# Performance work log

Measured on AMD Instinct MI355X. Metric: run time of the kernel, lower is better.

The kernel has to match this reference:

```python
import jax, jax.numpy as jnp
import numpy as np

B, T, S, D, H, F = 4, 1024, 1024, 1024, 16, 4096
NEG = jnp.float32(-1e9)


def _ln(x, g, b):
    m = jnp.mean(x, axis=-1, keepdims=True)
    v = jnp.mean((x - m) ** 2, axis=-1, keepdims=True)
    return (x - m) * jax.lax.rsqrt(v + 1e-5) * g + b


def _mha(q, k, v, wq, bq, wk, bk, wv, bv, wo, bo, scale, mask, causal, sbias):
    Bq, Tq, Dq = q.shape
    Sk = k.shape[1]
    dk = Dq // H
    Q = (q @ wq.T + bq).reshape(Bq, Tq, H, dk).transpose(0, 2, 1, 3)  # [B,H,T,dk]
    K = (k @ wk.T + bk).reshape(Bq, Sk, H, dk).transpose(0, 2, 1, 3)  # [B,H,S,dk]
    V = (v @ wv.T + bv).reshape(Bq, Sk, H, dk).transpose(0, 2, 1, 3)
    s = jnp.einsum('bhtd,bhsd->bhts', Q, K) / jnp.sqrt(jnp.float32(dk))
    if sbias is not None:
        s = s + scale * sbias[:, None, None, :]
    if mask is not None:
        s = jnp.where(mask == 0, NEG, s)
    if causal is not None:
        s = jnp.where(causal == 0, NEG, s)
    a = jax.nn.softmax(s, axis=-1)
    o = jnp.einsum('bhts,bhsd->bhtd', a, V).transpose(0, 2, 1, 3).reshape(Bq, Tq, Dq)
    return o @ wo.T + bo


def setup_inputs():
    key = jax.random.key(0)
    ks = jax.random.split(key, 16)
    r = lambda i, shape, s=0.02: jax.random.normal(ks[i], shape, dtype=jnp.float32) * s
    z = lambda *shape: jnp.zeros(shape, jnp.float32)
    o = lambda *shape: jnp.ones(shape, jnp.float32)
    inp = dict(
        x=r(0, (B, T, D), 1.0),
        memory=r(1, (B, S, D), 1.0),
        sentence_bias=r(2, (B, S), 1.0),
        trg_mask=jnp.ones((B, 1, 1, T), jnp.int32),
        trg_causal_mask=jnp.tril(jnp.ones((T, T), jnp.int32))[None, None],
        src_mask=jnp.ones((B, 1, 1, S), jnp.int32),
        sa_wq=r(3, (D, D)), sa_bq=z(D), sa_wk=r(4, (D, D)), sa_bk=z(D),
        sa_wv=r(5, (D, D)), sa_bv=z(D), sa_wo=r(6, (D, D)), sa_bo=z(D),
        sa_scale=jnp.float32(0.1),
        ca_wq=r(7, (D, D)), ca_bq=z(D), ca_wk=r(8, (D, D)), ca_bk=z(D),
        ca_wv=r(9, (D, D)), ca_bv=z(D), ca_wo=r(10, (D, D)), ca_bo=z(D),
        ca_scale=jnp.float32(0.1),
        ln1_g=o(D), ln1_b=z(D), ln2_g=o(D), ln2_b=z(D), ln3_g=o(D), ln3_b=z(D),
        ffn_w1=r(11, (F, D)), ffn_b1=z(F), ffn_w2=r(12, (D, F)), ffn_b2=z(D),
    )
    return inp


def reference(x, memory, trg_mask, trg_causal_mask, src_mask, sentence_bias,
              sa_wq, sa_bq, sa_wk, sa_bk, sa_wv, sa_bv, sa_wo, sa_bo, sa_scale,
              ca_wq, ca_bq, ca_wk, ca_bk, ca_wv, ca_bv, ca_wo, ca_bo, ca_scale,
              ln1_g, ln1_b, ln2_g, ln2_b, ln3_g, ln3_b,
              ffn_w1, ffn_b1, ffn_w2, ffn_b2):
    # Faithful quirk: Q comes from normed x, K/V from raw residual stream.
    x = x + _mha(_ln(x, ln1_g, ln1_b), x, x,
                 sa_wq, sa_bq, sa_wk, sa_bk, sa_wv, sa_bv, sa_wo, sa_bo,
                 sa_scale, trg_mask, trg_causal_mask, None)
    x = x + _mha(_ln(x, ln2_g, ln2_b), memory, memory,
                 ca_wq, ca_bq, ca_wk, ca_bk, ca_wv, ca_bv, ca_wo, ca_bo,
                 ca_scale, src_mask, None, sentence_bias)
    h = _ln(x, ln3_g, ln3_b)
    x = x + (jax.nn.relu(h @ ffn_w1.T + ffn_b1) @ ffn_w2.T + ffn_b2)
    return x
```

## Files before the change

kernel.cpp:

```cpp
#include <hip/hip_runtime.h>
#include <hip/hip_bf16.h>
#include <cmath>
#include <stdint.h>

typedef __hip_bfloat16 bf16;
typedef __attribute__((ext_vector_type(8))) __bf16 bf16x8;
typedef __attribute__((ext_vector_type(8))) unsigned short u16x8;
typedef __attribute__((ext_vector_type(4))) float f32x4;

__device__ __forceinline__ void gld16(const void* g, const void* l)
{
    __builtin_amdgcn_global_load_lds(
        (const __attribute__((address_space(1))) unsigned int*)(unsigned long long)g,
        (__attribute__((address_space(3))) unsigned int*)(unsigned int)(unsigned long long)l,
        16, 0, 0);
}

struct CvtSrcs { const float* p[24]; };

__global__ __launch_bounds__(256) void cvt_all(
    CvtSrcs s, bf16* __restrict__ dst,
    const float* __restrict__ lg, const float* __restrict__ lb,
    bf16* __restrict__ lnout)
{
    const int t = threadIdx.x;
    const int i = (blockIdx.x * 256 + t) * 8;
    const int seg = i >> 20;
    const float* sp = s.p[seg] + (i & 1048575);
    const float4 a = *(const float4*)(sp);
    const float4 b = *(const float4*)(sp + 4);
    const float v[8] = {a.x, a.y, a.z, a.w, b.x, b.y, b.z, b.w};
    bf16 tmp[8];
#pragma unroll
    for (int j = 0; j < 8; ++j) tmp[j] = __float2bfloat16(v[j]);
    *(uint4*)(dst + i) = *(const uint4*)tmp;

    if (seg < 4) {
        float s1 = 0.f, s2 = 0.f;
#pragma unroll
        for (int j = 0; j < 8; ++j) { s1 += v[j]; s2 += v[j] * v[j]; }
#pragma unroll
        for (int off = 32; off > 0; off >>= 1) {
            s1 += __shfl_xor(s1, off, 64);
            s2 += __shfl_xor(s2, off, 64);
        }
        __shared__ float r1[4], r2[4];
        const int w = t >> 6;
        if ((t & 63) == 0) { r1[w] = s1; r2[w] = s2; }
        __syncthreads();
        const int rw = (w >> 1) * 2;
        s1 = r1[rw] + r1[rw + 1];
        s2 = r2[rw] + r2[rw + 1];
        const float mean = s1 * (1.f / 1024.f);
        const float var  = s2 * (1.f / 1024.f) - mean * mean;
        const float rstd = rsqrtf(var + 1e-5f);
        bf16 lt[8];
        const int c0 = i & 1023;
#pragma unroll
        for (int j = 0; j < 8; ++j)
            lt[j] = __float2bfloat16((v[j] - mean) * rstd * lg[c0 + j] + lb[c0 + j]);
        *(uint4*)(lnout + i) = *(const uint4*)lt;
    }
}

enum {
    EPI_QSCALE = 0,
    EPI_KV = 1,
    EPI_RELU = 2,
    EPI_RES_F32_F32OUT = 3,
    EPI_PART = 4
};

template <int EPI>
__device__ __forceinline__ void gemm_bt_body(
    unsigned short* __restrict__ sAp, unsigned short* __restrict__ sBp,
    const bf16* __restrict__ A, const bf16* __restrict__ W,
    const float* __restrict__ bias, const float* __restrict__ bias2,
    const float* __restrict__ res, void* __restrict__ out,
    int N, int Kiter, int Kstride, int bx)
{
    const int t  = threadIdx.x;
    const int l  = t & 63;
    const int w  = t >> 6;
    const int wv = w * 64;
    const int wr = w >> 1;
    const int wc = w & 1;
    const int lm = l & 15;
    const int kq = l >> 4;
    const int rx = lm & 7;

    const int xcd = bx & 7;
    const int ib  = bx >> 3;
    const int bm  = xcd * 4 + (ib & 3);
    const int bn  = ib >> 2;

    const bf16* gA = A + (size_t)(bm * 128 + (t >> 3)) * Kstride
                       + ((t & 7) ^ ((t >> 3) & 7)) * 8;
    const bf16* gB = W + (size_t)(bn * 64 + (t >> 3)) * Kstride
                       + ((t & 7) ^ ((t >> 3) & 7)) * 8;

#define SQA_B(slot, kt, j)                                      \
    gld16(gA + (size_t)((j) * 32) * Kstride + (kt) * 64,        \
          sAp + (slot) * 8192 + ((j) * 256 + wv) * 8)
#define SQB_B(slot, kt, j)                                      \
    gld16(gB + (size_t)((j) * 32) * Kstride + (kt) * 64,        \
          sBp + (slot) * 4096 + ((j) * 256 + wv) * 8)

    bf16x8 af[4][2], bg[2][2];

#define READ_A_B(s_, mh, kk)                                                \
    do {                                                                    \
        _Pragma("unroll")                                                   \
        for (int m2 = 0; m2 < 2; ++m2) {                                    \
            const int mi = (mh) * 2 + m2;                                   \
            const int lr = wr * 64 + mi * 16 + lm;                          \
            const int sl = (((kk) << 2) | kq) ^ rx;                         \
            af[mi][kk] = __builtin_bit_cast(bf16x8,                         \
                *(const u16x8*)(sAp + (s_) * 8192 + lr * 64 + sl * 8));     \
        }                                                                   \
    } while (0)
#define READ_B_B(s_, kk)                                                    \
    do {                                                                    \
        _Pragma("unroll")                                                   \
        for (int ni = 0; ni < 2; ++ni) {                                    \
            const int lr = wc * 32 + ni * 16 + lm;                          \
            const int sl = (((kk) << 2) | kq) ^ rx;                         \
            bg[ni][kk] = __builtin_bit_cast(bf16x8,                         \
                *(const u16x8*)(sBp + (s_) * 4096 + lr * 64 + sl * 8));     \
        }                                                                   \
    } while (0)
#define MFMA_PH_B(mh, kk)                                                   \
    do {                                                                    \
        __builtin_amdgcn_s_setprio(1);                                      \
        _Pragma("unroll")                                                   \
        for (int m2 = 0; m2 < 2; ++m2)                                      \
            _Pragma("unroll")                                               \
            for (int ni = 0; ni < 2; ++ni)                                  \
                acc[(mh) * 2 + m2][ni] =                                    \
                    __builtin_amdgcn_mfma_f32_16x16x32_bf16(                \
                        af[(mh) * 2 + m2][kk], bg[ni][kk],                  \
                        acc[(mh) * 2 + m2][ni], 0, 0, 0);                   \
        __builtin_amdgcn_s_setprio(0);                                      \
    } while (0)
#define BARRIER_B() do { __builtin_amdgcn_s_barrier();                      \
                         __builtin_amdgcn_sched_barrier(0); } while (0)
#define WAITV0_B() asm volatile("s_waitcnt vmcnt(0)" ::: "memory")

    f32x4 acc[4][2] = {};
    const int NT = Kiter >> 6;

    SQB_B(0, 0, 0); SQB_B(0, 0, 1);
    SQA_B(0, 0, 0); SQA_B(0, 0, 1); SQA_B(0, 0, 2); SQA_B(0, 0, 3);

    for (int tt = 0; tt < NT; ++tt) {
        const int s = tt & 1, d = s ^ 1, kn = tt + 1;
        WAITV0_B(); BARRIER_B();
        if (kn < NT) {
            SQB_B(d, kn, 0); SQB_B(d, kn, 1);
            SQA_B(d, kn, 0); SQA_B(d, kn, 1); SQA_B(d, kn, 2); SQA_B(d, kn, 3);
        }
        READ_A_B(s, 0, 0); READ_B_B(s, 0);
        MFMA_PH_B(0, 0);
        READ_A_B(s, 1, 0);
        MFMA_PH_B(1, 0);
        READ_A_B(s, 1, 1); READ_B_B(s, 1);
        MFMA_PH_B(1, 1);
        READ_A_B(s, 0, 1);
        MFMA_PH_B(0, 1);
    }
#undef SQA_B
#undef SQB_B
#undef READ_A_B
#undef READ_B_B
#undef MFMA_PH_B
#undef BARRIER_B
#undef WAITV0_B

    if (EPI == EPI_RELU) {
        __syncthreads();
        unsigned short* scr = sBp + w * 2048;
#pragma unroll
        for (int ni = 0; ni < 2; ++ni) {
            const int col = bn * 64 + wc * 32 + ni * 16 + lm;
            const float bv = bias[col];
            const int c  = ni * 2 + (lm >> 3);
            const int ci = lm & 7;
#pragma unroll
            for (int mi = 0; mi < 4; ++mi)
#pragma unroll
                for (int r = 0; r < 4; ++r) {
                    const int row = mi * 16 + kq * 4 + r;
                    const float v = fmaxf(acc[mi][ni][r] + bv, 0.f);
                    scr[row * 32 + ((c ^ (row & 3)) * 8) + ci] =
                        __builtin_bit_cast(unsigned short, (__bf16)v);
                }
        }
        asm volatile("s_waitcnt lgkmcnt(0)" ::: "memory");
#pragma unroll
        for (int it = 0; it < 4; ++it) {
            const int row = it * 16 + (l >> 2);
            const int lc  = l & 3;
            const u16x8 vv = *(const u16x8*)&scr[row * 32 + ((lc ^ (row & 3)) * 8)];
            const int Crow = bm * 128 + wr * 64 + row;
            const int Ccol = bn * 64 + wc * 32 + lc * 8;
            *(u16x8*)((bf16*)out + (size_t)Crow * N + Ccol) = vv;
        }
        return;
    }

#pragma unroll
    for (int ni = 0; ni < 2; ++ni) {
        const int col = bn * 64 + wc * 32 + ni * 16 + lm;
        float bv = 0.f;
        if (EPI == EPI_KV) bv = (col < 1024) ? bias[col] : bias2[col - 1024];
        else bv = bias[col];
#pragma unroll
        for (int mi = 0; mi < 4; ++mi) {
#pragma unroll
            for (int r = 0; r < 4; ++r) {
                const int row = bm * 128 + wr * 64 + mi * 16 + kq * 4 + r;
                float v = acc[mi][ni][r] + bv;
                if (EPI == EPI_QSCALE) v *= 0.125f;
                if (EPI == EPI_KV) {
                    if (col < 1024) {
                        ((bf16*)out)[(size_t)row * 1024 + col] = __float2bfloat16(v);
                    } else {
                        const int ch = col - 1024;
                        const size_t idx = (size_t)4 * 1048576 +
                            ((size_t)((row >> 10) * 16 + (ch >> 6)) * 64 + (ch & 63)) * 1024
                            + (row & 1023);
                        ((bf16*)out)[idx] = __float2bfloat16(v);
                    }
                } else if (EPI == EPI_RES_F32_F32OUT) {
                    const size_t idx = (size_t)row * N + col;
                    ((float*)out)[idx] = v + res[idx];
                } else {
                    ((bf16*)out)[(size_t)row * N + col] = __float2bfloat16(v);
                }
            }
        }
    }
}

template <int EPI>
__global__ __launch_bounds__(256, 3) void gemm_bt(
    const bf16* __restrict__ A, const bf16* __restrict__ W,
    const float* __restrict__ bias, const float* __restrict__ bias2,
    const float* __restrict__ res, void* __restrict__ out,
    int M, int N, int Kiter, int Kstride)
{
    __shared__ __align__(16) unsigned short sA[2 * 128 * 64];
    __shared__ __align__(16) unsigned short sB[2 * 64 * 64];
    gemm_bt_body<EPI>(sA, sB, A, W, bias, bias2, res, out,
                      N, Kiter, Kstride, blockIdx.x);
}

__global__ __launch_bounds__(256, 3) void qkv_fused(
    const bf16* __restrict__ Aq, const bf16* __restrict__ Wq,
    const float* __restrict__ bq, bf16* __restrict__ Qb,
    const bf16* __restrict__ Akv, const bf16* __restrict__ Wkv,
    const float* __restrict__ bk, const float* __restrict__ bv,
    bf16* __restrict__ Kb)
{
    __shared__ __align__(16) unsigned short sA[2 * 128 * 64];
    __shared__ __align__(16) unsigned short sB[2 * 64 * 64];
    const int bx = blockIdx.x;
    if (bx < 512)
        gemm_bt_body<EPI_QSCALE>(sA, sB, Aq, Wq, bq, nullptr, nullptr, Qb,
                                 1024, 1024, 1024, bx);
    else
        gemm_bt_body<EPI_KV>(sA, sB, Akv, Wkv, bk, bv, nullptr, Kb,
                             2048, 1024, 1024, bx - 512);
}

template <bool CAUSAL, bool SBIAS>
__global__ __launch_bounds__(256, 2) void flash_attn(
    const bf16* __restrict__ Q, const bf16* __restrict__ K,
    const bf16* __restrict__ Vt, bf16* __restrict__ O,
    const float* __restrict__ sbias, const float* __restrict__ scale_ptr)
{
    __shared__ __align__(16) unsigned short sK[2][64 * 64];
    __shared__ __align__(16) unsigned short sV[2][64 * 64];
    __shared__ __align__(16) unsigned short sP[4 * 32 * 72];

    const int t  = threadIdx.x;
    const int l  = t & 63;
    const int w  = t >> 6;
    const int wv = w * 64;
    const int lm = l & 15;
    const int kq = l >> 4;

    const int bh = blockIdx.x & 63;
    const int qb = blockIdx.x >> 6;
    const int h  = bh & 15;
    const int b  = bh >> 4;

    const int tb = qb * 128 + w * 32;
    const size_t qrow0 = (size_t)(b * 1024 + tb) * 1024 + h * 64;

    bf16x8 qf[2][2];
#pragma unroll
    for (int mi = 0; mi < 2; ++mi)
#pragma unroll
        for (int kk = 0; kk < 2; ++kk)
            qf[mi][kk] = __builtin_bit_cast(bf16x8,
                *(const u16x8*)(Q + qrow0 + (size_t)(mi * 16 + lm) * 1024 + kk * 32 + kq * 8));

    float cs = 0.f; const float* sb = nullptr;
    if (SBIAS) { cs = scale_ptr[0]; sb = sbias + b * 1024; }

    const bf16* gK = K  + (size_t)(b * 1024 + (t >> 3)) * 1024 + h * 64
                   + ((t & 7) ^ ((t >> 3) & 7)) * 8;
    const bf16* gV = Vt + (size_t)((b * 16 + h) * 64 + (t >> 3)) * 1024
                   + ((t & 7) ^ ((t >> 3) & 7)) * 8;
    __bf16* sPw = (__bf16*)sP + w * 32 * 72;

#define STAGE_KV(buf, s0r)                                                   \
    do {                                                                     \
        gld16(gK + (size_t)(s0r) * 1024,        &sK[buf][wv * 8]);           \
        gld16(gK + (size_t)((s0r) + 32) * 1024, &sK[buf][2048 + wv * 8]);    \
        gld16(gV + (s0r),                       &sV[buf][wv * 8]);           \
        gld16(gV + (s0r) + 32 * 1024,           &sV[buf][2048 + wv * 8]);    \
    } while (0)

    const int niter = CAUSAL ? (2 * qb + 2) : 16;

    STAGE_KV(0, 0);
    __syncthreads();

    f32x4 acc_o[2][4] = {};
    f32x4 l_run[2] = {};

    for (int it = 0; it < niter; ++it) {
        const int s0 = it * 64;
        const int cur = it & 1;

        if (it + 1 < niter) STAGE_KV(cur ^ 1, s0 + 64);

        f32x4 accs[2][4] = {};
#pragma unroll
        for (int ni = 0; ni < 4; ++ni)
#pragma unroll
            for (int kk = 0; kk < 2; ++kk) {
                const bf16x8 kf = __builtin_bit_cast(bf16x8,
                    *(const u16x8*)(&sK[cur][(ni * 16 + lm) * 64
                        + ((((kk << 2) | kq)) ^ (lm & 7)) * 8]));
#pragma unroll
                for (int mi = 0; mi < 2; ++mi)
                    accs[mi][ni] = __builtin_amdgcn_mfma_f32_16x16x32_bf16(
                        qf[mi][kk], kf, accs[mi][ni], 0, 0, 0);
            }

        if (SBIAS) {
#pragma unroll
            for (int ni = 0; ni < 4; ++ni) {
                const float sv = cs * sb[s0 + ni * 16 + lm];
#pragma unroll
                for (int mi = 0; mi < 2; ++mi)
#pragma unroll
                    for (int r = 0; r < 4; ++r) accs[mi][ni][r] += sv;
            }
        }
        if (CAUSAL && (s0 + 63 > tb)) {
#pragma unroll
            for (int ni = 0; ni < 4; ++ni) {
                const int s = s0 + ni * 16 + lm;
#pragma unroll
                for (int mi = 0; mi < 2; ++mi)
#pragma unroll
                    for (int r = 0; r < 4; ++r)
                        if (s > tb + mi * 16 + kq * 4 + r) accs[mi][ni][r] = -1e30f;
            }
        }

#pragma unroll
        for (int mi = 0; mi < 2; ++mi)
#pragma unroll
            for (int ni = 0; ni < 4; ++ni)
#pragma unroll
                for (int r = 0; r < 4; ++r) {
                    const float e = __expf(accs[mi][ni][r]);
                    l_run[mi][r] += e;
                    sPw[(mi * 16 + kq * 4 + r) * 72 + ni * 16 + lm] = (__bf16)e;
                }

#pragma unroll
        for (int kk = 0; kk < 2; ++kk) {
            bf16x8 pf[2];
#pragma unroll
            for (int mi = 0; mi < 2; ++mi)
                pf[mi] = __builtin_bit_cast(bf16x8,
                    *(const u16x8*)(sPw + (mi * 16 + lm) * 72 + kk * 32 + kq * 8));
#pragma unroll
            for (int di = 0; di < 4; ++di) {
                const bf16x8 vf = __builtin_bit_cast(bf16x8,
                    *(const u16x8*)(&sV[cur][(di * 16 + lm) * 64
                        + ((((kk << 2) | kq)) ^ (lm & 7)) * 8]));
#pragma unroll
                for (int mi = 0; mi < 2; ++mi)
                    acc_o[mi][di] = __builtin_amdgcn_mfma_f32_16x16x32_bf16(
                        pf[mi], vf, acc_o[mi][di], 0, 0, 0);
            }
        }

        __syncthreads();
    }
#undef STAGE_KV

#pragma unroll
    for (int mi = 0; mi < 2; ++mi) {
        f32x4 lt = l_run[mi];
#pragma unroll
        for (int x = 1; x < 16; x <<= 1)
#pragma unroll
            for (int r = 0; r < 4; ++r) lt[r] += __shfl_xor(lt[r], x, 64);
#pragma unroll
        for (int r = 0; r < 4; ++r) lt[r] = 1.f / lt[r];
#pragma unroll
        for (int di = 0; di < 4; ++di)
#pragma unroll
            for (int r = 0; r < 4; ++r) {
                const size_t idx = (size_t)(b * 1024 + tb + mi * 16 + kq * 4 + r) * 1024
                                 + h * 64 + di * 16 + lm;
                O[idx] = __float2bfloat16(acc_o[mi][di][r] * lt[r]);
            }
    }
}

__global__ __launch_bounds__(256) void ln_kernel(
    const float* __restrict__ xin, const float* __restrict__ g,
    const float* __restrict__ bta, bf16* __restrict__ out)
{
    const int row = blockIdx.x;
    const int t = threadIdx.x;
    const size_t base = (size_t)row * 1024 + t * 4;

    const float4 f = *(const float4*)(xin + base);
    const float v[4] = {f.x, f.y, f.z, f.w};
    float s1 = v[0] + v[1] + v[2] + v[3];
    float s2 = v[0]*v[0] + v[1]*v[1] + v[2]*v[2] + v[3]*v[3];
#pragma unroll
    for (int off = 32; off > 0; off >>= 1) {
        s1 += __shfl_xor(s1, off, 64);
        s2 += __shfl_xor(s2, off, 64);
    }
    __shared__ float r1[4], r2[4];
    if ((t & 63) == 0) { r1[t >> 6] = s1; r2[t >> 6] = s2; }
    __syncthreads();
    s1 = r1[0] + r1[1] + r1[2] + r1[3];
    s2 = r2[0] + r2[1] + r2[2] + r2[3];
    const float mean = s1 * (1.f / 1024.f);
    const float var  = s2 * (1.f / 1024.f) - mean * mean;
    const float rstd = rsqrtf(var + 1e-5f);
#pragma unroll
    for (int j = 0; j < 4; ++j) {
        const int c = t * 4 + j;
        out[base + j] = __float2bfloat16((v[j] - mean) * rstd * g[c] + bta[c]);
    }
}

extern "C" void kernel_launch(void* const* d_in, const int* in_sizes, int n_in,
                              void* d_out, int out_size, void* d_ws, size_t ws_size,
                              hipStream_t stream)
{
    const float* x       = (const float*)d_in[0];
    const float* memory  = (const float*)d_in[1];
    const float* sbias   = (const float*)d_in[2];
    const float* sa_bq = (const float*)d_in[7];
    const float* sa_bk = (const float*)d_in[9];
    const float* sa_bv = (const float*)d_in[11];
    const float* sa_bo = (const float*)d_in[13];
    const float* ca_bq = (const float*)d_in[16];
    const float* ca_bk = (const float*)d_in[18];
    const float* ca_bv = (const float*)d_in[20];
    const float* ca_bo = (const float*)d_in[22];
    const float* ca_scale = (const float*)d_in[23];
    const float* ln1_g = (const float*)d_in[24]; const float* ln1_b = (const float*)d_in[25];
    const float* ln2_g = (const float*)d_in[26]; const float* ln2_b = (const float*)d_in[27];
    const float* ln3_g = (const float*)d_in[28]; const float* ln3_b = (const float*)d_in[29];
    const float* b1 = (const float*)d_in[31];
    const float* b2 = (const float*)d_in[33];

    char* ws = (char*)d_ws;
    const size_t MB = (size_t)1 << 20;
    float* x1    = (float*)(ws + 0 * MB);
    float* x2    = (float*)(ws + 16 * MB);
    bf16* lnbuf  = (bf16*)(ws + 32 * MB);
    bf16* Qb     = (bf16*)(ws + 40 * MB);
    bf16* Kb     = (bf16*)(ws + 48 * MB);
    bf16* Vtb    = (bf16*)(ws + 56 * MB);
    bf16* Ob     = (bf16*)(ws + 64 * MB);
    bf16* ffnmid = (bf16*)(ws + 40 * MB);
    bf16* wx     = (bf16*)(ws + 72 * MB);
    bf16* wmem   = (bf16*)(ws + 80 * MB);
    bf16* bw     = (bf16*)(ws + 88 * MB);
    bf16* b_sa_wq = bw + 0 * 1048576, *b_sa_wk = bw + 1 * 1048576;
    bf16* b_sa_wo = bw + 3 * 1048576;
    bf16* b_ca_wq = bw + 4 * 1048576, *b_ca_wk = bw + 5 * 1048576;
    bf16* b_ca_wo = bw + 7 * 1048576;
    bf16* b_w1   = (bf16*)(ws + 104 * MB);
    bf16* b_w2   = (bf16*)(ws + 112 * MB);

    const int M = 4096;
    dim3 blk256(256);
    const dim3 gQ(512);
    const dim3 gQKV(1536);
    const dim3 gFA(512);
    const dim3 gF1(2048);

    CvtSrcs cs;
    for (int c = 0; c < 4; ++c) {
        cs.p[c]      = x + (size_t)c * 1048576;
        cs.p[4 + c]  = memory + (size_t)c * 1048576;
        cs.p[16 + c] = (const float*)d_in[30] + (size_t)c * 1048576;
        cs.p[20 + c] = (const float*)d_in[32] + (size_t)c * 1048576;
    }
    cs.p[8]  = (const float*)d_in[6];
    cs.p[9]  = (const float*)d_in[8];
    cs.p[10] = (const float*)d_in[10];
    cs.p[11] = (const float*)d_in[12];
    cs.p[12] = (const float*)d_in[15];
    cs.p[13] = (const float*)d_in[17];
    cs.p[14] = (const float*)d_in[19];
    cs.p[15] = (const float*)d_in[21];
    cvt_all<<<24 * 1048576 / 2048, blk256, 0, stream>>>(
        cs, wx, ln1_g, ln1_b, lnbuf);

    qkv_fused<<<gQKV, blk256, 0, stream>>>(
        lnbuf, b_sa_wq, sa_bq, Qb, wx, b_sa_wk, sa_bk, sa_bv, Kb);
    flash_attn<true, false><<<gFA, blk256, 0, stream>>>(Qb, Kb, Vtb, Ob, nullptr, nullptr);
    gemm_bt<EPI_RES_F32_F32OUT><<<gQ, blk256, 0, stream>>>(
        Ob, b_sa_wo, sa_bo, nullptr, x, x1, M, 1024, 1024, 1024);

    ln_kernel<<<4096, blk256, 0, stream>>>(x1, ln2_g, ln2_b, lnbuf);
    qkv_fused<<<gQKV, blk256, 0, stream>>>(
        lnbuf, b_ca_wq, ca_bq, Qb, wmem, b_ca_wk, ca_bk, ca_bv, Kb);
    flash_attn<false, true><<<gFA, blk256, 0, stream>>>(Qb, Kb, Vtb, Ob, sbias, ca_scale);
    gemm_bt<EPI_RES_F32_F32OUT><<<gQ, blk256, 0, stream>>>(
        Ob, b_ca_wo, ca_bo, nullptr, x1, x2, M, 1024, 1024, 1024);

    ln_kernel<<<4096, blk256, 0, stream>>>(x2, ln3_g, ln3_b, lnbuf);
    gemm_bt<EPI_RELU><<<gF1, blk256, 0, stream>>>(
        lnbuf, b_w1, b1, nullptr, nullptr, ffnmid, M, 4096, 1024, 1024);
    gemm_bt<EPI_RES_F32_F32OUT><<<gQ, blk256, 0, stream>>>(
        ffnmid, b_w2, b2, nullptr, x2, d_out, M, 1024, 4096, 4096);
}
```

Before: 452.5 us.

## Enlarge GEMM tile to 128x128 with 4x4 MFMA per wave and LDS-staged epilogue

The shared GEMM body moves from a 128x64 to a 128x128 output tile. Each wave now computes a 64x64 sub-tile with a 4x4 grid of MFMAs per k-step, which raises arithmetic intensity per LDS read and halves the grid sizes. The Q-scale and K paths now share the swizzled-LDS vectorized store epilogue that ReLU already used, and the residual and V-transpose paths get their own branches. In exchange, doubling the B tile in LDS and the accumulators per thread cuts occupancy from 3 to 2 blocks per CU. The grids are also halved, which lowers parallelism for the smaller GEMMs.

After: 453.5 us. No clear change (+0.2%).

```diff
diff --git a/kernel.cpp b/kernel.cpp
--- a/kernel.cpp
+++ b/kernel.cpp
@@ -96,7 +96,7 @@
 
     const bf16* gA = A + (size_t)(bm * 128 + (t >> 3)) * Kstride
                        + ((t & 7) ^ ((t >> 3) & 7)) * 8;
-    const bf16* gB = W + (size_t)(bn * 64 + (t >> 3)) * Kstride
+    const bf16* gB = W + (size_t)(bn * 128 + (t >> 3)) * Kstride
                        + ((t & 7) ^ ((t >> 3) & 7)) * 8;
 
 #define SQA_B(slot, kt, j)                                      \
@@ -104,69 +104,62 @@
           sAp + (slot) * 8192 + ((j) * 256 + wv) * 8)
 #define SQB_B(slot, kt, j)                                      \
     gld16(gB + (size_t)((j) * 32) * Kstride + (kt) * 64,        \
-          sBp + (slot) * 4096 + ((j) * 256 + wv) * 8)
-
-    bf16x8 af[4][2], bg[2][2];
-
-#define READ_A_B(s_, mh, kk)                                                \
+          sBp + (slot) * 8192 + ((j) * 256 + wv) * 8)
+
+    bf16x8 af[4], bg[4];
+
+#define READ_A_B(s_, kk)                                                    \
     do {                                                                    \
         _Pragma("unroll")                                                   \
-        for (int m2 = 0; m2 < 2; ++m2) {                                    \
-            const int mi = (mh) * 2 + m2;                                   \
+        for (int mi = 0; mi < 4; ++mi) {                                    \
             const int lr = wr * 64 + mi * 16 + lm;                          \
             const int sl = (((kk) << 2) | kq) ^ rx;                         \
-            af[mi][kk] = __builtin_bit_cast(bf16x8,                         \
+            af[mi] = __builtin_bit_cast(bf16x8,                             \
                 *(const u16x8*)(sAp + (s_) * 8192 + lr * 64 + sl * 8));     \
         }                                                                   \
     } while (0)
 #define READ_B_B(s_, kk)                                                    \
     do {                                                                    \
         _Pragma("unroll")                                                   \
-        for (int ni = 0; ni < 2; ++ni) {                                    \
-            const int lr = wc * 32 + ni * 16 + lm;                          \
+        for (int ni = 0; ni < 4; ++ni) {                                    \
+            const int lr = wc * 64 + ni * 16 + lm;                          \
             const int sl = (((kk) << 2) | kq) ^ rx;                         \
-            bg[ni][kk] = __builtin_bit_cast(bf16x8,                         \
-                *(const u16x8*)(sBp + (s_) * 4096 + lr * 64 + sl * 8));     \
+            bg[ni] = __builtin_bit_cast(bf16x8,                             \
+                *(const u16x8*)(sBp + (s_) * 8192 + lr * 64 + sl * 8));     \
         }                                                                   \
     } while (0)
-#define MFMA_PH_B(mh, kk)                                                   \
+#define MFMA_PH_B()                                                         \
     do {                                                                    \
         __builtin_amdgcn_s_setprio(1);                                      \
         _Pragma("unroll")                                                   \
-        for (int m2 = 0; m2 < 2; ++m2)                                      \
+        for (int mi = 0; mi < 4; ++mi)                                      \
             _Pragma("unroll")                                               \
-            for (int ni = 0; ni < 2; ++ni)                                  \
-                acc[(mh) * 2 + m2][ni] =                                    \
-                    __builtin_amdgcn_mfma_f32_16x16x32_bf16(                \
-                        af[(mh) * 2 + m2][kk], bg[ni][kk],                  \
-                        acc[(mh) * 2 + m2][ni], 0, 0, 0);                   \
+            for (int ni = 0; ni < 4; ++ni)                                  \
+                acc[mi][ni] = __builtin_amdgcn_mfma_f32_16x16x32_bf16(      \
+                    af[mi], bg[ni], acc[mi][ni], 0, 0, 0);                  \
         __builtin_amdgcn_s_setprio(0);                                      \
     } while (0)
 #define BARRIER_B() do { __builtin_amdgcn_s_barrier();                      \
                          __builtin_amdgcn_sched_barrier(0); } while (0)
 #define WAITV0_B() asm volatile("s_waitcnt vmcnt(0)" ::: "memory")
 
-    f32x4 acc[4][2] = {};
+    f32x4 acc[4][4] = {};
     const int NT = Kiter >> 6;
 
-    SQB_B(0, 0, 0); SQB_B(0, 0, 1);
+    SQB_B(0, 0, 0); SQB_B(0, 0, 1); SQB_B(0, 0, 2); SQB_B(0, 0, 3);
     SQA_B(0, 0, 0); SQA_B(0, 0, 1); SQA_B(0, 0, 2); SQA_B(0, 0, 3);
 
     for (int tt = 0; tt < NT; ++tt) {
         const int s = tt & 1, d = s ^ 1, kn = tt + 1;
         WAITV0_B(); BARRIER_B();
         if (kn < NT) {
-            SQB_B(d, kn, 0); SQB_B(d, kn, 1);
+            SQB_B(d, kn, 0); SQB_B(d, kn, 1); SQB_B(d, kn, 2); SQB_B(d, kn, 3);
             SQA_B(d, kn, 0); SQA_B(d, kn, 1); SQA_B(d, kn, 2); SQA_B(d, kn, 3);
         }
-        READ_A_B(s, 0, 0); READ_B_B(s, 0);
-        MFMA_PH_B(0, 0);
-        READ_A_B(s, 1, 0);
-        MFMA_PH_B(1, 0);
-        READ_A_B(s, 1, 1); READ_B_B(s, 1);
-        MFMA_PH_B(1, 1);
-        READ_A_B(s, 0, 1);
-        MFMA_PH_B(0, 1);
+        READ_A_B(s, 0); READ_B_B(s, 0);
+        MFMA_PH_B();
+        READ_A_B(s, 1); READ_B_B(s, 1);
+        MFMA_PH_B();
     }
 #undef SQA_B
 #undef SQB_B
@@ -176,12 +169,51 @@
 #undef BARRIER_B
 #undef WAITV0_B
 
-    if (EPI == EPI_RELU) {
+    if (EPI == EPI_RES_F32_F32OUT) {
+#pragma unroll
+        for (int ni = 0; ni < 4; ++ni) {
+            const int col = bn * 128 + wc * 64 + ni * 16 + lm;
+            const float bv = bias[col];
+#pragma unroll
+            for (int mi = 0; mi < 4; ++mi)
+#pragma unroll
+                for (int r = 0; r < 4; ++r) {
+                    const int row = bm * 128 + wr * 64 + mi * 16 + kq * 4 + r;
+                    const size_t idx = (size_t)row * N + col;
+                    ((float*)out)[idx] = acc[mi][ni][r] + bv + res[idx];
+                }
+        }
+        return;
+    }
+
+    if (EPI == EPI_KV && bn >= 8) {
+#pragma unroll
+        for (int ni = 0; ni < 4; ++ni) {
+            const int col = bn * 128 + wc * 64 + ni * 16 + lm;
+            const float bv = bias2[col - 1024];
+#pragma unroll
+            for (int mi = 0; mi < 4; ++mi)
+#pragma unroll
+                for (int r = 0; r < 4; ++r) {
+                    const int row = bm * 128 + wr * 64 + mi * 16 + kq * 4 + r;
+                    const float v = acc[mi][ni][r] + bv;
+                    const int ch = col - 1024;
+                    const size_t idx = (size_t)4 * 1048576 +
+                        ((size_t)((row >> 10) * 16 + (ch >> 6)) * 64 + (ch & 63)) * 1024
+                        + (row & 1023);
+                    ((bf16*)out)[idx] = __float2bfloat16(v);
+                }
+        }
+        return;
+    }
+
+    {
+        const int outN = (EPI == EPI_KV) ? 1024 : N;
         __syncthreads();
-        unsigned short* scr = sBp + w * 2048;
-#pragma unroll
-        for (int ni = 0; ni < 2; ++ni) {
-            const int col = bn * 64 + wc * 32 + ni * 16 + lm;
+        unsigned short* scr = sAp + w * 4096;
+#pragma unroll
+        for (int ni = 0; ni < 4; ++ni) {
+            const int col = bn * 128 + wc * 64 + ni * 16 + lm;
             const float bv = bias[col];
             const int c  = ni * 2 + (lm >> 3);
             const int ci = lm & 7;
@@ -190,72 +222,40 @@
 #pragma unroll
                 for (int r = 0; r < 4; ++r) {
                     const int row = mi * 16 + kq * 4 + r;
-                    const float v = fmaxf(acc[mi][ni][r] + bv, 0.f);
-                    scr[row * 32 + ((c ^ (row & 3)) * 8) + ci] =
+                    float v = acc[mi][ni][r] + bv;
+                    if (EPI == EPI_QSCALE) v *= 0.125f;
+                    if (EPI == EPI_RELU) v = fmaxf(v, 0.f);
+                    scr[row * 64 + ((c ^ (row & 7)) * 8) + ci] =
                         __builtin_bit_cast(unsigned short, (__bf16)v);
                 }
         }
         asm volatile("s_waitcnt lgkmcnt(0)" ::: "memory");
 #pragma unroll
-        for (int it = 0; it < 4; ++it) {
-            const int row = it * 16 + (l >> 2);
-            const int lc  = l & 3;
-            const u16x8 vv = *(const u16x8*)&scr[row * 32 + ((lc ^ (row & 3)) * 8)];
+        for (int it = 0; it < 8; ++it) {
+            const int row = it * 8 + (l >> 3);
+            const int lc  = l & 7;
+            const u16x8 vv = *(const u16x8*)&scr[row * 64 + ((lc ^ (row & 7)) * 8)];
             const int Crow = bm * 128 + wr * 64 + row;
-            const int Ccol = bn * 64 + wc * 32 + lc * 8;
-            *(u16x8*)((bf16*)out + (size_t)Crow * N + Ccol) = vv;
-        }
-        return;
-    }
-
-#pragma unroll
-    for (int ni = 0; ni < 2; ++ni) {
-        const int col = bn * 64 + wc * 32 + ni * 16 + lm;
-        float bv = 0.f;
-        if (EPI == EPI_KV) bv = (col < 1024) ? bias[col] : bias2[col - 1024];
-        else bv = bias[col];
-#pragma unroll
-        for (int mi = 0; mi < 4; ++mi) {
-#pragma unroll
-            for (int r = 0; r < 4; ++r) {
-                const int row = bm * 128 + wr * 64 + mi * 16 + kq * 4 + r;
-                float v = acc[mi][ni][r] + bv;
-                if (EPI == EPI_QSCALE) v *= 0.125f;
-                if (EPI == EPI_KV) {
-                    if (col < 1024) {
-                        ((bf16*)out)[(size_t)row * 1024 + col] = __float2bfloat16(v);
-                    } else {
-                        const int ch = col - 1024;
-                        const size_t idx = (size_t)4 * 1048576 +
-                            ((size_t)((row >> 10) * 16 + (ch >> 6)) * 64 + (ch & 63)) * 1024
-                            + (row & 1023);
-                        ((bf16*)out)[idx] = __float2bfloat16(v);
-                    }
-                } else if (EPI == EPI_RES_F32_F32OUT) {
-                    const size_t idx = (size_t)row * N + col;
-                    ((float*)out)[idx] = v + res[idx];
-                } else {
-                    ((bf16*)out)[(size_t)row * N + col] = __float2bfloat16(v);
-                }
-            }
+            const int Ccol = bn * 128 + wc * 64 + lc * 8;
+            *(u16x8*)((bf16*)out + (size_t)Crow * outN + Ccol) = vv;
         }
     }
 }
 
 template <int EPI>
-__global__ __launch_bounds__(256, 3) void gemm_bt(
+__global__ __launch_bounds__(256, 2) void gemm_bt(
     const bf16* __restrict__ A, const bf16* __restrict__ W,
     const float* __restrict__ bias, const float* __restrict__ bias2,
     const float* __restrict__ res, void* __restrict__ out,
     int M, int N, int Kiter, int Kstride)
 {
     __shared__ __align__(16) unsigned short sA[2 * 128 * 64];
-    __shared__ __align__(16) unsigned short sB[2 * 64 * 64];
+    __shared__ __align__(16) unsigned short sB[2 * 128 * 64];
     gemm_bt_body<EPI>(sA, sB, A, W, bias, bias2, res, out,
                       N, Kiter, Kstride, blockIdx.x);
 }
 
-__global__ __launch_bounds__(256, 3) void qkv_fused(
+__global__ __launch_bounds__(256, 2) void qkv_fused(
     const bf16* __restrict__ Aq, const bf16* __restrict__ Wq,
     const float* __restrict__ bq, bf16* __restrict__ Qb,
     const bf16* __restrict__ Akv, const bf16* __restrict__ Wkv,
@@ -263,14 +263,14 @@
     bf16* __restrict__ Kb)
 {
     __shared__ __align__(16) unsigned short sA[2 * 128 * 64];
-    __shared__ __align__(16) unsigned short sB[2 * 64 * 64];
+    __shared__ __align__(16) unsigned short sB[2 * 128 * 64];
     const int bx = blockIdx.x;
-    if (bx < 512)
+    if (bx < 256)
         gemm_bt_body<EPI_QSCALE>(sA, sB, Aq, Wq, bq, nullptr, nullptr, Qb,
                                  1024, 1024, 1024, bx);
     else
         gemm_bt_body<EPI_KV>(sA, sB, Akv, Wkv, bk, bv, nullptr, Kb,
-                             2048, 1024, 1024, bx - 512);
+                             2048, 1024, 1024, bx - 256);
 }
 
 template <bool CAUSAL, bool SBIAS>
@@ -503,10 +503,10 @@
 
     const int M = 4096;
     dim3 blk256(256);
-    const dim3 gQ(512);
-    const dim3 gQKV(1536);
+    const dim3 gQ(256);
+    const dim3 gQKV(768);
     const dim3 gFA(512);
-    const dim3 gF1(2048);
+    const dim3 gF1(1024);
 
     CvtSrcs cs;
     for (int c = 0; c < 4; ++c) {
```

## Use 128x128 tile GEMM for FFN up-projection and loop cvt kernel over chunks

Applied to the files above, without the earlier changes.

Adds a new GEMM kernel with a 128x128 output tile per block (4x4 MFMA fragments per wave) and uses it for the FFN1 ReLU GEMM, halving the grid and raising arithmetic intensity per LDS load. The ReLU epilogue moves into this kernel with a wider swizzled LDS staging buffer. Separately, the convert/LayerNorm prologue kernel now processes four chunks per block with a smaller grid, reducing block launch overhead at the cost of extra barriers. The larger tile raises register and LDS use, so occupancy drops to 2 blocks per CU.

Measured after the change: 462.0 us. +2.1%, slower.

```diff
diff --git a/kernel.cpp b/kernel.cpp
--- a/kernel.cpp
+++ b/kernel.cpp
@@ -24,42 +24,47 @@
     bf16* __restrict__ lnout)
 {
     const int t = threadIdx.x;
-    const int i = (blockIdx.x * 256 + t) * 8;
-    const int seg = i >> 20;
-    const float* sp = s.p[seg] + (i & 1048575);
-    const float4 a = *(const float4*)(sp);
-    const float4 b = *(const float4*)(sp + 4);
-    const float v[8] = {a.x, a.y, a.z, a.w, b.x, b.y, b.z, b.w};
-    bf16 tmp[8];
-#pragma unroll
-    for (int j = 0; j < 8; ++j) tmp[j] = __float2bfloat16(v[j]);
-    *(uint4*)(dst + i) = *(const uint4*)tmp;
-
-    if (seg < 4) {
-        float s1 = 0.f, s2 = 0.f;
-#pragma unroll
-        for (int j = 0; j < 8; ++j) { s1 += v[j]; s2 += v[j] * v[j]; }
-#pragma unroll
-        for (int off = 32; off > 0; off >>= 1) {
-            s1 += __shfl_xor(s1, off, 64);
-            s2 += __shfl_xor(s2, off, 64);
+    __shared__ float r1[4], r2[4];
+#pragma unroll
+    for (int it = 0; it < 4; ++it) {
+        const int chunk = blockIdx.x + it * 3072;
+        const int i = chunk * 2048 + t * 8;
+        const int seg = i >> 20;
+        const float* sp = s.p[seg] + (i & 1048575);
+        const float4 a = *(const float4*)(sp);
+        const float4 b = *(const float4*)(sp + 4);
+        const float v[8] = {a.x, a.y, a.z, a.w, b.x, b.y, b.z, b.w};
+        bf16 tmp[8];
+#pragma unroll
+        for (int j = 0; j < 8; ++j) tmp[j] = __float2bfloat16(v[j]);
+        *(uint4*)(dst + i) = *(const uint4*)tmp;
+
+        if (seg < 4) {
+            float s1 = 0.f, s2 = 0.f;
+#pragma unroll
+            for (int j = 0; j < 8; ++j) { s1 += v[j]; s2 += v[j] * v[j]; }
+#pragma unroll
+            for (int off = 32; off > 0; off >>= 1) {
+                s1 += __shfl_xor(s1, off, 64);
+                s2 += __shfl_xor(s2, off, 64);
+            }
+            const int w = t >> 6;
+            __syncthreads();
+            if ((t & 63) == 0) { r1[w] = s1; r2[w] = s2; }
+            __syncthreads();
+            const int rw = (w >> 1) * 2;
+            s1 = r1[rw] + r1[rw + 1];
+            s2 = r2[rw] + r2[rw + 1];
+            const float mean = s1 * (1.f / 1024.f);
+            const float var  = s2 * (1.f / 1024.f) - mean * mean;
+            const float rstd = rsqrtf(var + 1e-5f);
+            bf16 lt[8];
+            const int c0 = i & 1023;
+#pragma unroll
+            for (int j = 0; j < 8; ++j)
+                lt[j] = __float2bfloat16((v[j] - mean) * rstd * lg[c0 + j] + lb[c0 + j]);
+            *(uint4*)(lnout + i) = *(const uint4*)lt;
         }
-        __shared__ float r1[4], r2[4];
-        const int w = t >> 6;
-        if ((t & 63) == 0) { r1[w] = s1; r2[w] = s2; }
-        __syncthreads();
-        const int rw = (w >> 1) * 2;
-        s1 = r1[rw] + r1[rw + 1];
-        s2 = r2[rw] + r2[rw + 1];
-        const float mean = s1 * (1.f / 1024.f);
-        const float var  = s2 * (1.f / 1024.f) - mean * mean;
-        const float rstd = rsqrtf(var + 1e-5f);
-        bf16 lt[8];
-        const int c0 = i & 1023;
-#pragma unroll
-        for (int j = 0; j < 8; ++j)
-            lt[j] = __float2bfloat16((v[j] - mean) * rstd * lg[c0 + j] + lb[c0 + j]);
-        *(uint4*)(lnout + i) = *(const uint4*)lt;
     }
 }
 
@@ -72,7 +77,7 @@
 };
 
 template <int EPI>
-__device__ __forceinline__ void gemm_bt_body(
+__device__ __forceinline__ void body64(
     unsigned short* __restrict__ sAp, unsigned short* __restrict__ sBp,
     const bf16* __restrict__ A, const bf16* __restrict__ W,
     const float* __restrict__ bias, const float* __restrict__ bias2,
@@ -176,38 +181,6 @@
 #undef BARRIER_B
 #undef WAITV0_B
 
-    if (EPI == EPI_RELU) {
-        __syncthreads();
-        unsigned short* scr = sBp + w * 2048;
-#pragma unroll
-        for (int ni = 0; ni < 2; ++ni) {
-            const int col = bn * 64 + wc * 32 + ni * 16 + lm;
-            const float bv = bias[col];
-            const int c  = ni * 2 + (lm >> 3);
-            const int ci = lm & 7;
-#pragma unroll
-            for (int mi = 0; mi < 4; ++mi)
-#pragma unroll
-                for (int r = 0; r < 4; ++r) {
-                    const int row = mi * 16 + kq * 4 + r;
-                    const float v = fmaxf(acc[mi][ni][r] + bv, 0.f);
-                    scr[row * 32 + ((c ^ (row & 3)) * 8) + ci] =
-                        __builtin_bit_cast(unsigned short, (__bf16)v);
-                }
-        }
-        asm volatile("s_waitcnt lgkmcnt(0)" ::: "memory");
-#pragma unroll
-        for (int it = 0; it < 4; ++it) {
-            const int row = it * 16 + (l >> 2);
-            const int lc  = l & 3;
-            const u16x8 vv = *(const u16x8*)&scr[row * 32 + ((lc ^ (row & 3)) * 8)];
-            const int Crow = bm * 128 + wr * 64 + row;
-            const int Ccol = bn * 64 + wc * 32 + lc * 8;
-            *(u16x8*)((bf16*)out + (size_t)Crow * N + Ccol) = vv;
-        }
-        return;
-    }
-
 #pragma unroll
     for (int ni = 0; ni < 2; ++ni) {
         const int col = bn * 64 + wc * 32 + ni * 16 + lm;
@@ -243,7 +216,7 @@
 }
 
 template <int EPI>
-__global__ __launch_bounds__(256, 3) void gemm_bt(
+__global__ __launch_bounds__(256, 3) void gemm_n64(
     const bf16* __restrict__ A, const bf16* __restrict__ W,
     const float* __restrict__ bias, const float* __restrict__ bias2,
     const float* __restrict__ res, void* __restrict__ out,
@@ -251,8 +224,8 @@
 {
     __shared__ __align__(16) unsigned short sA[2 * 128 * 64];
     __shared__ __align__(16) unsigned short sB[2 * 64 * 64];
-    gemm_bt_body<EPI>(sA, sB, A, W, bias, bias2, res, out,
-                      N, Kiter, Kstride, blockIdx.x);
+    body64<EPI>(sA, sB, A, W, bias, bias2, res, out,
+                N, Kiter, Kstride, blockIdx.x);
 }
 
 __global__ __launch_bounds__(256, 3) void qkv_fused(
@@ -266,11 +239,142 @@
     __shared__ __align__(16) unsigned short sB[2 * 64 * 64];
     const int bx = blockIdx.x;
     if (bx < 512)
-        gemm_bt_body<EPI_QSCALE>(sA, sB, Aq, Wq, bq, nullptr, nullptr, Qb,
-                                 1024, 1024, 1024, bx);
+        body64<EPI_QSCALE>(sA, sB, Aq, Wq, bq, nullptr, nullptr, Qb,
+                           1024, 1024, 1024, bx);
     else
-        gemm_bt_body<EPI_KV>(sA, sB, Akv, Wkv, bk, bv, nullptr, Kb,
-                             2048, 1024, 1024, bx - 512);
+        body64<EPI_KV>(sA, sB, Akv, Wkv, bk, bv, nullptr, Kb,
+                       2048, 1024, 1024, bx - 512);
+}
+
+template <int EPI>
+__global__ __launch_bounds__(256, 2) void gemm_n128(
+    const bf16* __restrict__ A, const bf16* __restrict__ W,
+    const float* __restrict__ bias, void* __restrict__ out,
+    int N, int Kiter, int Kstride)
+{
+    __shared__ __align__(16) unsigned short sAp[2 * 128 * 64];
+    __shared__ __align__(16) unsigned short sBp[2 * 128 * 64];
+
+    const int t  = threadIdx.x;
+    const int l  = t & 63;
+    const int w  = t >> 6;
+    const int wv = w * 64;
+    const int wr = w >> 1;
+    const int wc = w & 1;
+    const int lm = l & 15;
+    const int kq = l >> 4;
+    const int rx = lm & 7;
+
+    const int bx  = blockIdx.x;
+    const int xcd = bx & 7;
+    const int ib  = bx >> 3;
+    const int bm  = xcd * 4 + (ib & 3);
+    const int bn  = ib >> 2;
+
+    const bf16* gA = A + (size_t)(bm * 128 + (t >> 3)) * Kstride
+                       + ((t & 7) ^ ((t >> 3) & 7)) * 8;
+    const bf16* gB = W + (size_t)(bn * 128 + (t >> 3)) * Kstride
+                       + ((t & 7) ^ ((t >> 3) & 7)) * 8;
+
+#define SQA_C(slot, kt, j)                                      \
+    gld16(gA + (size_t)((j) * 32) * Kstride + (kt) * 64,        \
+          sAp + (slot) * 8192 + ((j) * 256 + wv) * 8)
+#define SQB_C(slot, kt, j)                                      \
+    gld16(gB + (size_t)((j) * 32) * Kstride + (kt) * 64,        \
+          sBp + (slot) * 8192 + ((j) * 256 + wv) * 8)
+
+    bf16x8 af[4], bg[4];
+
+#define READ_A_C(s_, kk)                                                    \
+    do {                                                                    \
+        _Pragma("unroll")                                                   \
+        for (int mi = 0; mi < 4; ++mi) {                                    \
+            const int lr = wr * 64 + mi * 16 + lm;                          \
+            const int sl = (((kk) << 2) | kq) ^ rx;                         \
+            af[mi] = __builtin_bit_cast(bf16x8,                             \
+                *(const u16x8*)(sAp + (s_) * 8192 + lr * 64 + sl * 8));     \
+        }                                                                   \
+    } while (0)
+#define READ_B_C(s_, kk)                                                    \
+    do {                                                                    \
+        _Pragma("unroll")                                                   \
+        for (int ni = 0; ni < 4; ++ni) {                                    \
+            const int lr = wc * 64 + ni * 16 + lm;                          \
+            const int sl = (((kk) << 2) | kq) ^ rx;                         \
+            bg[ni] = __builtin_bit_cast(bf16x8,                             \
+                *(const u16x8*)(sBp + (s_) * 8192 + lr * 64 + sl * 8));     \
+        }                                                                   \
+    } while (0)
+#define MFMA_PH_C()                                                         \
+    do {                                                                    \
+        __builtin_amdgcn_s_setprio(1);                                      \
+        _Pragma("unroll")                                                   \
+        for (int mi = 0; mi < 4; ++mi)                                      \
+            _Pragma("unroll")                                               \
+            for (int ni = 0; ni < 4; ++ni)                                  \
+                acc[mi][ni] = __builtin_amdgcn_mfma_f32_16x16x32_bf16(      \
+                    af[mi], bg[ni], acc[mi][ni], 0, 0, 0);                  \
+        __builtin_amdgcn_s_setprio(0);                                      \
+    } while (0)
+#define BARRIER_C() do { __builtin_amdgcn_s_barrier();                      \
+                         __builtin_amdgcn_sched_barrier(0); } while (0)
+#define WAITV0_C() asm volatile("s_waitcnt vmcnt(0)" ::: "memory")
+
+    f32x4 acc[4][4] = {};
+    const int NT = Kiter >> 6;
+
+    SQB_C(0, 0, 0); SQB_C(0, 0, 1); SQB_C(0, 0, 2); SQB_C(0, 0, 3);
+    SQA_C(0, 0, 0); SQA_C(0, 0, 1); SQA_C(0, 0, 2); SQA_C(0, 0, 3);
+
+    for (int tt = 0; tt < NT; ++tt) {
+        const int s = tt & 1, d = s ^ 1, kn = tt + 1;
+        WAITV0_C(); BARRIER_C();
+        if (kn < NT) {
+            SQB_C(d, kn, 0); SQB_C(d, kn, 1); SQB_C(d, kn, 2); SQB_C(d, kn, 3);
+            SQA_C(d, kn, 0); SQA_C(d, kn, 1); SQA_C(d, kn, 2); SQA_C(d, kn, 3);
+        }
+        READ_A_C(s, 0); READ_B_C(s, 0);
+        MFMA_PH_C();
+        READ_A_C(s, 1); READ_B_C(s, 1);
+        MFMA_PH_C();
+    }
+#undef SQA_C
+#undef SQB_C
+#undef READ_A_C
+#undef READ_B_C
+#undef MFMA_PH_C
+#undef BARRIER_C
+#undef WAITV0_C
+
+    __syncthreads();
+    unsigned short* scr = sAp + w * 4096;
+#pragma unroll
+    for (int ni = 0; ni < 4; ++ni) {
+        const int col = bn * 128 + wc * 64 + ni * 16 + lm;
+        const float bv = bias[col];
+        const int c  = ni * 2 + (lm >> 3);
+        const int ci = lm & 7;
+#pragma unroll
+        for (int mi = 0; mi < 4; ++mi)
+#pragma unroll
+            for (int r = 0; r < 4; ++r) {
+                const int row = mi * 16 + kq * 4 + r;
+                float v = acc[mi][ni][r] + bv;
+                if (EPI == EPI_RELU) v = fmaxf(v, 0.f);
+                scr[row * 64 + ((c ^ (row & 7)) * 8) + ci] =
+                    __builtin_bit_cast(unsigned short, (__bf16)v);
+            }
+    }
+    asm volatile("s_waitcnt lgkmcnt(0)" ::: "memory");
+#pragma unroll
+    for (int it = 0; it < 8; ++it) {
+        const int row = it * 8 + (l >> 3);
+        const int lc  = l & 7;
+        const u16x8 vv = *(const u16x8*)&scr[row * 64 + ((lc ^ (row & 7)) * 8)];
+        const int Crow = bm * 128 + wr * 64 + row;
+        const int Ccol = bn * 128 + wc * 64 + lc * 8;
+        *(u16x8*)((bf16*)out + (size_t)Crow * N + Ccol) = vv;
+    }
 }
 
 template <bool CAUSAL, bool SBIAS>
@@ -506,7 +610,7 @@
     const dim3 gQ(512);
     const dim3 gQKV(1536);
     const dim3 gFA(512);
-    const dim3 gF1(2048);
+    const dim3 gF1(1024);
 
     CvtSrcs cs;
     for (int c = 0; c < 4; ++c) {
@@ -523,25 +627,24 @@
     cs.p[13] = (const float*)d_in[17];
     cs.p[14] = (const float*)d_in[19];
     cs.p[15] = (const float*)d_in[21];
-    cvt_all<<<24 * 1048576 / 2048, blk256, 0, stream>>>(
-        cs, wx, ln1_g, ln1_b, lnbuf);
+    cvt_all<<<3072, blk256, 0, stream>>>(cs, wx, ln1_g, ln1_b, lnbuf);
 
     qkv_fused<<<gQKV, blk256, 0, stream>>>(
         lnbuf, b_sa_wq, sa_bq, Qb, wx, b_sa_wk, sa_bk, sa_bv, Kb);
     flash_attn<true, false><<<gFA, blk256, 0, stream>>>(Qb, Kb, Vtb, Ob, nullptr, nullptr);
-    gemm_bt<EPI_RES_F32_F32OUT><<<gQ, blk256, 0, stream>>>(
+    gemm_n64<EPI_RES_F32_F32OUT><<<gQ, blk256, 0, stream>>>(
         Ob, b_sa_wo, sa_bo, nullptr, x, x1, M, 1024, 1024, 1024);
 
     ln_kernel<<<4096, blk256, 0, stream>>>(x1, ln2_g, ln2_b, lnbuf);
     qkv_fused<<<gQKV, blk256, 0, stream>>>(
         lnbuf, b_ca_wq, ca_bq, Qb, wmem, b_ca_wk, ca_bk, ca_bv, Kb);
     flash_attn<false, true><<<gFA, blk256, 0, stream>>>(Qb, Kb, Vtb, Ob, sbias, ca_scale);
-    gemm_bt<EPI_RES_F32_F32OUT><<<gQ, blk256, 0, stream>>>(
+    gemm_n64<EPI_RES_F32_F32OUT><<<gQ, blk256, 0, stream>>>(
         Ob, b_ca_wo, ca_bo, nullptr, x1, x2, M, 1024, 1024, 1024);
 
     ln_kernel<<<4096, blk256, 0, stream>>>(x2, ln3_g, ln3_b, lnbuf);
-    gemm_bt<EPI_RELU><<<gF1, blk256, 0, stream>>>(
-        lnbuf, b_w1, b1, nullptr, nullptr, ffnmid, M, 4096, 1024, 1024);
-    gemm_bt<EPI_RES_F32_F32OUT><<<gQ, blk256, 0, stream>>>(
+    gemm_n128<EPI_RELU><<<gF1, blk256, 0, stream>>>(
+        lnbuf, b_w1, b1, ffnmid, 4096, 1024, 1024);
+    gemm_n64<EPI_RES_F32_F32OUT><<<gQ, blk256, 0, stream>>>(
         ffnmid, b_w2, b2, nullptr, x2, d_out, M, 1024, 4096, 4096);
 }
```
